# Performance work log

Hardware: AMD Instinct MI355X
Metric: run time of the kernel (lower is better)

The kernel has to match this reference:

```python
import jax, jax.numpy as jnp
import numpy as np

INF = 1.0e10
EPS = 1e-12

def setup_inputs() -> dict:
    key = jax.random.key(0)
    k1, k2 = jax.random.split(key)
    B, N, A = 512, 16384, 64
    return {
        "residue_ca_pos": jax.random.normal(k1, (B, N, 3), dtype=jnp.float32) * 10.0,
        "residue_mask": jnp.ones((B, N), dtype=jnp.float32),
        "atom_pos": jax.random.normal(k2, (B, A, 3), dtype=jnp.float32) * 10.0,
        "atom_mask": jnp.ones((B, A), dtype=jnp.float32),
        "max_p": 1,
        "top_k": 4096,
    }

def reference(residue_ca_pos, residue_mask, atom_pos, atom_mask, max_p, top_k):
    # ligand centroid per batch: [B, 3]
    centroid = atom_pos.sum(-2) / atom_mask.sum(-1, keepdims=True)
    # distance from centroid to each residue Ca, invalid residues pushed to +inf
    diff = centroid[:, None, :] - residue_ca_pos            # [B, N, 3]
    dists = jnp.sqrt(jnp.sum(diff * diff, axis=-1) + EPS) + (1.0 - residue_mask) * INF
    # k smallest distances -> neighbor indices [B, top_k]
    _, nbr_indices = jax.lax.top_k(-dists, top_k)
    rows = jnp.arange(residue_mask.shape[0])[:, None]       # [B, 1]
    # scatter writes building the masks (faithful to torch scatter_ with constants)
    residue_spatial_mask = residue_mask.at[rows, nbr_indices].set(0.0)
    residue_spatial_mask_esm = (1.0 - residue_mask).at[rows, nbr_indices].set(32.0)
    return residue_spatial_mask, residue_spatial_mask_esm
```

## Files before the change

kernel.cpp:

```cpp
#include <hip/hip_runtime.h>

#pragma clang fp contract(off)

#define B_     512
#define N_     16384
#define A_     64
#define TPB    1024
#define CAP    2048
#define NCHUNK 16
#define NBUF   3

#define AS1 __attribute__((address_space(1)))
#define AS3 __attribute__((address_space(3)))

__device__ __forceinline__ void gl2lds16(const float* g, float* l) {
    __builtin_amdgcn_global_load_lds((const AS1 unsigned int*)g,
                                     (AS3 unsigned int*)l, 16, 0, 0);
}

__global__ __launch_bounds__(TPB) void fused_kernel(
    const float* __restrict__ pos,   const float* __restrict__ mask,
    const float* __restrict__ apos,  const float* __restrict__ amask,
    const int*   __restrict__ topk_ptr,
    float* __restrict__ out0, float* __restrict__ out1)
{
#pragma clang fp contract(off)
    __shared__ __align__(16) float stage[NBUF][4096];
    __shared__ unsigned       hist[2048];
    __shared__ unsigned       hist2[32];
    __shared__ unsigned       cand_bits[CAP];
    __shared__ unsigned short cand_idx[CAP];
    __shared__ unsigned char  sel_flags[CAP];
    __shared__ float          s_atoms[A_ * 3 + A_];
    __shared__ float          s_c[3];
    __shared__ unsigned s_B11, s_less11, s_P16, s_j, s_ncand, s_k;

    const int tid = threadIdx.x;
    const int b   = blockIdx.x;
    const float* __restrict__ p = pos  + (size_t)b * N_ * 3;
    const float* __restrict__ m = mask + (size_t)b * N_;

    hist[tid]        = 0u;
    hist[tid + 1024] = 0u;
    if (tid < 32) hist2[tid] = 0u;
    if (tid < 256)
        s_atoms[tid] = (tid < 192) ? apos[(size_t)b * 192 + tid]
                                   : amask[(size_t)b * 64 + (tid - 192)];
    if (tid == 0) {
        s_ncand = 0u;
        int kk = *topk_ptr;
        if (kk < 0)  kk = 0;
        if (kk > N_) kk = N_;
        s_k = (unsigned)kk;
    }

    {
        const float* g0 = (tid < 768) ? (p + tid * 4)            : (m + (tid - 768) * 4);
        const float* g1 = (tid < 768) ? (p + 3072 + tid * 4)     : (m + 1024 + (tid - 768) * 4);
        const float* g2 = (tid < 768) ? (p + 2 * 3072 + tid * 4) : (m + 2 * 1024 + (tid - 768) * 4);
        gl2lds16(g0, &stage[0][tid * 4]);
        gl2lds16(g1, &stage[1][tid * 4]);
        gl2lds16(g2, &stage[2][tid * 4]);
    }
    __syncthreads();

    if (tid < 64) {
        float comp = 0.0f, ms = 0.0f;
        if (tid < 3) {
            comp = s_atoms[tid];
            for (int a = 1; a < A_; ++a) comp += s_atoms[a * 3 + tid];
        }
        if (tid == 3) {
            const float* am = s_atoms + 192;
            float r0 = am[0], r1 = am[1], r2 = am[2], r3 = am[3];
            float r4 = am[4], r5 = am[5], r6 = am[6], r7 = am[7];
            for (int i = 8; i < A_; i += 8) {
                r0 += am[i + 0]; r1 += am[i + 1]; r2 += am[i + 2]; r3 += am[i + 3];
                r4 += am[i + 4]; r5 += am[i + 5]; r6 += am[i + 6]; r7 += am[i + 7];
            }
            ms = ((r0 + r1) + (r2 + r3)) + ((r4 + r5) + (r6 + r7));
        }
        ms = __shfl(ms, 3, 64);
        if (tid < 3) s_c[tid] = comp / ms;
    }
    __syncthreads();

    const float cx = s_c[0], cy = s_c[1], cz = s_c[2];
    const unsigned k = s_k;

    unsigned rbits[NCHUNK];
    float    rm[NCHUNK];

#pragma unroll
    for (int c = 0; c < NCHUNK; ++c) {
        if (c <= NCHUNK - 3)      asm volatile("s_waitcnt vmcnt(2)" ::: "memory");
        else if (c == NCHUNK - 2) asm volatile("s_waitcnt vmcnt(1)" ::: "memory");
        else                      asm volatile("s_waitcnt vmcnt(0)" ::: "memory");
        __builtin_amdgcn_s_barrier();
        asm volatile("" ::: "memory");

        const float* buf = stage[c % NBUF];
        const float px = buf[3 * tid];
        const float py = buf[3 * tid + 1];
        const float pz = buf[3 * tid + 2];
        const float mm = buf[3072 + tid];

        float dx = cx - px, dy = cy - py, dz = cz - pz;
        float dx2 = dx * dx, dy2 = dy * dy, dz2 = dz * dz;
        float s = (dx2 + dy2) + dz2;
        s = s + 1e-12f;
        float d = sqrtf(s);
        d = d + (1.0f - mm) * 1e10f;
        const unsigned bits = __float_as_uint(d);
        rbits[c] = bits;
        rm[c]    = mm;
        atomicAdd(&hist[bits >> 21], 1u);

        asm volatile("s_waitcnt lgkmcnt(0)" ::: "memory");
        __builtin_amdgcn_s_barrier();
        asm volatile("" ::: "memory");
        if (c + NBUF < NCHUNK) {
            const float* g = (tid < 768)
                ? (p + (size_t)(c + NBUF) * 3072 + tid * 4)
                : (m + (size_t)(c + NBUF) * 1024 + (tid - 768) * 4);
            gl2lds16(g, &stage[c % NBUF][tid * 4]);
        }
    }
    __syncthreads();

    if (k > 0) {
        if (tid < 64) {
            unsigned s = 0;
#pragma unroll
            for (int i = 0; i < 32; ++i) s += hist[tid * 32 + i];
            unsigned incl = s;
#pragma unroll
            for (int off = 1; off < 64; off <<= 1) {
                unsigned v = (unsigned)__shfl_up((int)incl, off, 64);
                if (tid >= off) incl += v;
            }
            unsigned long long bal = __ballot(incl >= k);
            const int g = __ffsll(bal) - 1;
            const unsigned cum1 = (unsigned)__shfl((int)(incl - s), g, 64);

            unsigned h2 = (tid < 32) ? hist[g * 32 + tid] : 0u;
            unsigned incl2 = h2;
#pragma unroll
            for (int off = 1; off < 64; off <<= 1) {
                unsigned v = (unsigned)__shfl_up((int)incl2, off, 64);
                if (tid >= off) incl2 += v;
            }
            unsigned long long bal2 = __ballot(tid < 32 && (cum1 + incl2 >= k));
            const int sb = __ffsll(bal2) - 1;
            const unsigned cum2 = cum1 + (unsigned)__shfl((int)(incl2 - h2), sb, 64);
            if (tid == 0) { s_B11 = (unsigned)(g * 32 + sb); s_less11 = cum2; }
        }
        __syncthreads();
        const unsigned B11 = s_B11;

#pragma unroll
        for (int x = 0; x < NCHUNK; ++x) {
            const unsigned v = rbits[x] >> 16;
            if ((v >> 5) == B11) atomicAdd(&hist2[v & 31u], 1u);
        }
        __syncthreads();
        if (tid < 64) {
            unsigned h = (tid < 32) ? hist2[tid] : 0u;
            unsigned incl = h;
#pragma unroll
            for (int off = 1; off < 64; off <<= 1) {
                unsigned v = (unsigned)__shfl_up((int)incl, off, 64);
                if (tid >= off) incl += v;
            }
            const unsigned less11 = s_less11;
            unsigned long long bal = __ballot(tid < 32 && (less11 + incl >= k));
            const int sb = __ffsll(bal) - 1;
            const unsigned cumx = less11 + (unsigned)__shfl((int)(incl - h), sb, 64);
            if (tid == 0) { s_P16 = (B11 << 5) | (unsigned)sb; s_j = k - cumx; }
        }
        __syncthreads();
        const unsigned P16 = s_P16;
        const unsigned j   = s_j;

#pragma unroll
        for (int c2 = 0; c2 < NCHUNK; ++c2) {
            const unsigned bits = rbits[c2];
            if ((bits >> 16) == P16) {
                const unsigned w = atomicAdd(&s_ncand, 1u);
                if (w < CAP) {
                    cand_bits[w] = bits;
                    cand_idx[w]  = (unsigned short)(c2 * 1024 + tid);
                    rbits[c2] = 0xFFFF0000u | w;
                }
            }
        }
        __syncthreads();

        const unsigned cnum = min(s_ncand, (unsigned)CAP);
        for (unsigned t = tid; t < cnum; t += TPB) {
            const unsigned bt = cand_bits[t];
            const unsigned it = cand_idx[t];
            unsigned rank = 0;
            for (unsigned u = 0; u < cnum; ++u) {
                const unsigned bu = cand_bits[u];
                rank += (bu < bt) || (bu == bt && (unsigned)cand_idx[u] < it);
            }
            sel_flags[t] = (rank < j) ? (unsigned char)1 : (unsigned char)0;
        }
        __syncthreads();
    }

    const unsigned P16f = (k > 0) ? s_P16 : 0u;
#pragma unroll
    for (int c2 = 0; c2 < NCHUNK; ++c2) {
        const unsigned v   = rbits[c2];
        const unsigned v16 = v >> 16;
        bool sel = false;
        if (k > 0) {
            sel = (v16 == 0xFFFFu) ? (sel_flags[v & (CAP - 1u)] != 0)
                                   : (v16 < P16f);
        }
        const float mv = rm[c2];
        const size_t o = (size_t)b * N_ + (size_t)c2 * 1024 + tid;
        out0[o] = sel ? 0.0f  : mv;
        out1[o] = sel ? 32.0f : (1.0f - mv);
    }
}

extern "C" void kernel_launch(void* const* d_in, const int* in_sizes, int n_in,
                              void* d_out, int out_size, void* d_ws, size_t ws_size,
                              hipStream_t stream) {
    const float* pos   = (const float*)d_in[0];
    const float* rmask = (const float*)d_in[1];
    const float* apos  = (const float*)d_in[2];
    const float* amask = (const float*)d_in[3];
    const int*   topk  = (const int*)d_in[5];

    float* out0 = (float*)d_out;
    float* out1 = out0 + (size_t)B_ * N_;

    fused_kernel<<<B_, TPB, 0, stream>>>(pos, rmask, apos, amask, topk, out0, out1);
}
```

Measured before the change: 211.6 us.

## Give each wave a private double-buffered staging slice, dropping block barriers in load loop

```diff
diff --git a/kernel.cpp b/kernel.cpp
--- a/kernel.cpp
+++ b/kernel.cpp
@@ -2,13 +2,12 @@
 
 #pragma clang fp contract(off)
 
-#define B_     512
-#define N_     16384
-#define A_     64
-#define TPB    1024
-#define CAP    2048
-#define NCHUNK 16
-#define NBUF   3
+#define B_   512
+#define N_   16384
+#define A_   64
+#define TPB  1024
+#define NW   16
+#define CAP  2048
 
 #define AS1 __attribute__((address_space(1)))
 #define AS3 __attribute__((address_space(3)))
@@ -25,17 +24,18 @@
     float* __restrict__ out0, float* __restrict__ out1)
 {
 #pragma clang fp contract(off)
-    __shared__ __align__(16) float stage[NBUF][4096];
+    __shared__ __align__(16) float wbuf[NW][2][1024];
     __shared__ unsigned       hist[2048];
     __shared__ unsigned       hist2[32];
     __shared__ unsigned       cand_bits[CAP];
     __shared__ unsigned short cand_idx[CAP];
     __shared__ unsigned char  sel_flags[CAP];
     __shared__ float          s_atoms[A_ * 3 + A_];
-    __shared__ float          s_c[3];
     __shared__ unsigned s_B11, s_less11, s_P16, s_j, s_ncand, s_k;
 
     const int tid = threadIdx.x;
+    const int w   = tid >> 6;
+    const int l   = tid & 63;
     const int b   = blockIdx.x;
     const float* __restrict__ p = pos  + (size_t)b * N_ * 3;
     const float* __restrict__ m = mask + (size_t)b * N_;
@@ -53,24 +53,28 @@
         if (kk > N_) kk = N_;
         s_k = (unsigned)kk;
     }
-
+    __syncthreads();
+
+#define ISSUE_SUB(S, BUFIDX) do {                                          \
+        const float* ps_ = p + (size_t)(w * 1024 + (S) * 256) * 3;         \
+        float* dst_ = &wbuf[w][(BUFIDX)][0];                               \
+        gl2lds16(ps_ + 4 * l,        dst_ + 4 * l);                        \
+        gl2lds16(ps_ + 256 + 4 * l,  dst_ + 256 + 4 * l);                  \
+        gl2lds16(ps_ + 512 + 4 * l,  dst_ + 512 + 4 * l);                  \
+        gl2lds16(m + w * 1024 + (S) * 256 + 4 * l, dst_ + 768 + 4 * l);    \
+    } while (0)
+
+    ISSUE_SUB(0, 0);
+    ISSUE_SUB(1, 1);
+
+    float cx, cy, cz;
     {
-        const float* g0 = (tid < 768) ? (p + tid * 4)            : (m + (tid - 768) * 4);
-        const float* g1 = (tid < 768) ? (p + 3072 + tid * 4)     : (m + 1024 + (tid - 768) * 4);
-        const float* g2 = (tid < 768) ? (p + 2 * 3072 + tid * 4) : (m + 2 * 1024 + (tid - 768) * 4);
-        gl2lds16(g0, &stage[0][tid * 4]);
-        gl2lds16(g1, &stage[1][tid * 4]);
-        gl2lds16(g2, &stage[2][tid * 4]);
-    }
-    __syncthreads();
-
-    if (tid < 64) {
         float comp = 0.0f, ms = 0.0f;
-        if (tid < 3) {
-            comp = s_atoms[tid];
-            for (int a = 1; a < A_; ++a) comp += s_atoms[a * 3 + tid];
-        }
-        if (tid == 3) {
+        if (l < 3) {
+            comp = s_atoms[l];
+            for (int a = 1; a < A_; ++a) comp += s_atoms[a * 3 + l];
+        }
+        if (l == 3) {
             const float* am = s_atoms + 192;
             float r0 = am[0], r1 = am[1], r2 = am[2], r3 = am[3];
             float r4 = am[4], r5 = am[5], r6 = am[6], r7 = am[7];
@@ -81,50 +85,49 @@
             ms = ((r0 + r1) + (r2 + r3)) + ((r4 + r5) + (r6 + r7));
         }
         ms = __shfl(ms, 3, 64);
-        if (tid < 3) s_c[tid] = comp / ms;
-    }
-    __syncthreads();
-
-    const float cx = s_c[0], cy = s_c[1], cz = s_c[2];
+        const float cc = (l < 3) ? comp / ms : 0.0f;
+        cx = __shfl(cc, 0, 64);
+        cy = __shfl(cc, 1, 64);
+        cz = __shfl(cc, 2, 64);
+    }
+
     const unsigned k = s_k;
 
-    unsigned rbits[NCHUNK];
-    float    rm[NCHUNK];
-
-#pragma unroll
-    for (int c = 0; c < NCHUNK; ++c) {
-        if (c <= NCHUNK - 3)      asm volatile("s_waitcnt vmcnt(2)" ::: "memory");
-        else if (c == NCHUNK - 2) asm volatile("s_waitcnt vmcnt(1)" ::: "memory");
-        else                      asm volatile("s_waitcnt vmcnt(0)" ::: "memory");
-        __builtin_amdgcn_s_barrier();
-        asm volatile("" ::: "memory");
-
-        const float* buf = stage[c % NBUF];
-        const float px = buf[3 * tid];
-        const float py = buf[3 * tid + 1];
-        const float pz = buf[3 * tid + 2];
-        const float mm = buf[3072 + tid];
-
-        float dx = cx - px, dy = cy - py, dz = cz - pz;
-        float dx2 = dx * dx, dy2 = dy * dy, dz2 = dz * dz;
-        float s = (dx2 + dy2) + dz2;
-        s = s + 1e-12f;
-        float d = sqrtf(s);
-        d = d + (1.0f - mm) * 1e10f;
-        const unsigned bits = __float_as_uint(d);
-        rbits[c] = bits;
-        rm[c]    = mm;
-        atomicAdd(&hist[bits >> 21], 1u);
+    unsigned rbits[16];
+    float    rmv[16];
+
+#define DO_ELEM(S, J, PX, PY, PZ, MM) do {                                 \
+        float dx_ = cx - (PX), dy_ = cy - (PY), dz_ = cz - (PZ);           \
+        float s_ = (dx_ * dx_ + dy_ * dy_) + dz_ * dz_;                    \
+        s_ = s_ + 1e-12f;                                                  \
+        float d_ = sqrtf(s_);                                              \
+        d_ = d_ + (1.0f - (MM)) * 1e10f;                                   \
+        const unsigned bits_ = __float_as_uint(d_);                        \
+        rbits[(S) * 4 + (J)] = bits_;                                      \
+        rmv[(S) * 4 + (J)]   = (MM);                                       \
+        atomicAdd(&hist[bits_ >> 21], 1u);                                 \
+    } while (0)
+
+#pragma unroll
+    for (int s = 0; s < 4; ++s) {
+        if (s < 3) asm volatile("s_waitcnt vmcnt(4)" ::: "memory");
+        else       asm volatile("s_waitcnt vmcnt(0)" ::: "memory");
+        __builtin_amdgcn_sched_barrier(0);
+
+        const float* buf = &wbuf[w][s & 1][0];
+        const float4 q0 = *(const float4*)(buf + 12 * l);
+        const float4 q1 = *(const float4*)(buf + 12 * l + 4);
+        const float4 q2 = *(const float4*)(buf + 12 * l + 8);
+        const float4 mv = *(const float4*)(buf + 768 + 4 * l);
+
+        DO_ELEM(s, 0, q0.x, q0.y, q0.z, mv.x);
+        DO_ELEM(s, 1, q0.w, q1.x, q1.y, mv.y);
+        DO_ELEM(s, 2, q1.z, q1.w, q2.x, mv.z);
+        DO_ELEM(s, 3, q2.y, q2.z, q2.w, mv.w);
 
         asm volatile("s_waitcnt lgkmcnt(0)" ::: "memory");
-        __builtin_amdgcn_s_barrier();
-        asm volatile("" ::: "memory");
-        if (c + NBUF < NCHUNK) {
-            const float* g = (tid < 768)
-                ? (p + (size_t)(c + NBUF) * 3072 + tid * 4)
-                : (m + (size_t)(c + NBUF) * 1024 + (tid - 768) * 4);
-            gl2lds16(g, &stage[c % NBUF][tid * 4]);
-        }
+        __builtin_amdgcn_sched_barrier(0);
+        if (s + 2 < 4) ISSUE_SUB(s + 2, s & 1);
     }
     __syncthreads();
 
@@ -159,7 +162,7 @@
         const unsigned B11 = s_B11;
 
 #pragma unroll
-        for (int x = 0; x < NCHUNK; ++x) {
+        for (int x = 0; x < 16; ++x) {
             const unsigned v = rbits[x] >> 16;
             if ((v >> 5) == B11) atomicAdd(&hist2[v & 31u], 1u);
         }
@@ -183,14 +186,15 @@
         const unsigned j   = s_j;
 
 #pragma unroll
-        for (int c2 = 0; c2 < NCHUNK; ++c2) {
-            const unsigned bits = rbits[c2];
+        for (int x = 0; x < 16; ++x) {
+            const unsigned bits = rbits[x];
             if ((bits >> 16) == P16) {
-                const unsigned w = atomicAdd(&s_ncand, 1u);
-                if (w < CAP) {
-                    cand_bits[w] = bits;
-                    cand_idx[w]  = (unsigned short)(c2 * 1024 + tid);
-                    rbits[c2] = 0xFFFF0000u | w;
+                const unsigned wr = atomicAdd(&s_ncand, 1u);
+                if (wr < CAP) {
+                    cand_bits[wr] = bits;
+                    cand_idx[wr]  = (unsigned short)(w * 1024 + (x >> 2) * 256
+                                                     + 4 * l + (x & 3));
+                    rbits[x] = 0xFFFF0000u | wr;
                 }
             }
         }
@@ -212,18 +216,25 @@
 
     const unsigned P16f = (k > 0) ? s_P16 : 0u;
 #pragma unroll
-    for (int c2 = 0; c2 < NCHUNK; ++c2) {
-        const unsigned v   = rbits[c2];
-        const unsigned v16 = v >> 16;
-        bool sel = false;
-        if (k > 0) {
-            sel = (v16 == 0xFFFFu) ? (sel_flags[v & (CAP - 1u)] != 0)
-                                   : (v16 < P16f);
-        }
-        const float mv = rm[c2];
-        const size_t o = (size_t)b * N_ + (size_t)c2 * 1024 + tid;
-        out0[o] = sel ? 0.0f  : mv;
-        out1[o] = sel ? 32.0f : (1.0f - mv);
+    for (int s = 0; s < 4; ++s) {
+        float4 o0, o1;
+        float* o0p = &o0.x; float* o1p = &o1.x;
+#pragma unroll
+        for (int jj = 0; jj < 4; ++jj) {
+            const unsigned v   = rbits[s * 4 + jj];
+            const unsigned v16 = v >> 16;
+            bool sel = false;
+            if (k > 0) {
+                sel = (v16 == 0xFFFFu) ? (sel_flags[v & (CAP - 1u)] != 0)
+                                       : (v16 < P16f);
+            }
+            const float mvv = rmv[s * 4 + jj];
+            o0p[jj] = sel ? 0.0f  : mvv;
+            o1p[jj] = sel ? 32.0f : (1.0f - mvv);
+        }
+        const size_t o = (size_t)b * N_ + w * 1024 + s * 256 + 4 * l;
+        *(float4*)(out0 + o) = o0;
+        *(float4*)(out1 + o) = o1;
     }
 }
 
```

Measured after the change: 212.9 us. About the same (+0.6%).
